# Optimization experiments

Measured on AMD Instinct MI355X. Metric: run time of the kernel, lower is better.

Reference implementation:

```python
import jax, jax.numpy as jnp
import numpy as np

B, L, C, D, K = 32, 36864, 16, 512, 24


def setup_inputs() -> dict:
    key = jax.random.key(0)
    ks = jax.random.split(key, 5)
    x = jax.random.normal(ks[0], (B, L, C), jnp.float32)
    # offset-conv weights scaled small so predicted offsets are O(0.2) (kaiming-ish but tame)
    w_off = jax.random.normal(ks[1], (2 * K, C, K), jnp.float32) * 0.01
    b_off = jax.random.normal(ks[2], (2 * K,), jnp.float32) * 0.05
    w_def = jax.random.normal(ks[3], (D, C, K), jnp.float32) * (2.0 / (C * K)) ** 0.5
    b_def = jax.random.normal(ks[4], (D,), jnp.float32) * 0.05
    return {"x": x, "w_off": w_off, "b_off": b_off, "w_def": w_def, "b_def": b_def}


def reference(x, w_off, b_off, w_def, b_def):
    # x: [B, L, C] -> torch view [B, C, 1, L]; H == 1 throughout.
    Bn, Ln, Cn = x.shape
    twoK, _, Kn = w_off.shape
    Lout = Ln // Kn
    xc = jnp.transpose(x, (0, 2, 1))                 # [B, C, L]
    xk = xc.reshape(Bn, Cn, Lout, Kn)                # stride == kernel -> non-overlapping windows
    # offset conv: [B, 2K, Lout]
    off = jnp.einsum('bclk,ock->bol', xk, w_off) + b_off[None, :, None]
    off = off.reshape(Bn, Kn, 2, Lout)               # channel 2k -> dy, 2k+1 -> dx (torchvision layout)
    dy = jnp.transpose(off[:, :, 0, :], (0, 2, 1))   # [B, Lout, K]
    dx = jnp.transpose(off[:, :, 1, :], (0, 2, 1))   # [B, Lout, K]
    # sampling positions along width; base = w_out*K + k
    base = jnp.arange(Lout * Kn, dtype=x.dtype).reshape(Lout, Kn)
    px = base[None] + dx                             # [B, Lout, K]
    # height bilinear weight: with H=1, contribution at h=0 is max(0, 1-|dy|)
    wy = jnp.maximum(jnp.array(0, x.dtype), 1.0 - jnp.abs(dy))
    # width bilinear with zero padding (torchvision bilinear_interpolate semantics)
    valid = (px > -1.0) & (px < Ln)
    x0 = jnp.floor(px)
    lw = px - x0                                     # weight for right neighbor
    i0 = x0.astype(jnp.int32)
    i1 = i0 + 1
    m0 = (valid & (i0 >= 0) & (i0 < Ln)).astype(x.dtype)
    m1 = (valid & (i1 >= 0) & (i1 < Ln)).astype(x.dtype)
    i0c = jnp.broadcast_to(jnp.clip(i0, 0, Ln - 1).reshape(Bn, 1, Lout * Kn), (Bn, Cn, Lout * Kn))
    i1c = jnp.broadcast_to(jnp.clip(i1, 0, Ln - 1).reshape(Bn, 1, Lout * Kn), (Bn, Cn, Lout * Kn))
    v0 = jnp.take_along_axis(xc, i0c, axis=2).reshape(Bn, Cn, Lout, Kn)
    v1 = jnp.take_along_axis(xc, i1c, axis=2).reshape(Bn, Cn, Lout, Kn)
    val = (v0 * ((1.0 - lw) * m0)[:, None] + v1 * (lw * m1)[:, None]) * wy[:, None]  # [B,C,Lout,K]
    out = jnp.einsum('bclk,dck->bld', val, w_def) + b_def  # [B, Lout, D]
    return out
```

## Files before the change

kernel.cpp:

```cpp
#include <hip/hip_runtime.h>
#include <stdint.h>

#define BATCH 32
#define LLEN  36864
#define CCH   16
#define DOUT  512
#define KW    24
#define LOUT  1536
#define MROWS (BATCH * LOUT)
#define CK    384
#define TWOK  48

typedef float fx4 __attribute__((ext_vector_type(4)));
typedef float f32x4 __attribute__((ext_vector_type(4)));
typedef __bf16 bf16x8 __attribute__((ext_vector_type(8)));
typedef uint32_t u32x4 __attribute__((ext_vector_type(4)));

#define VMCNT(n)  asm volatile("s_waitcnt vmcnt(" #n ")" ::: "memory")
#define LGKMCNT0  asm volatile("s_waitcnt lgkmcnt(0)" ::: "memory")
#define SCHEDB    __builtin_amdgcn_sched_barrier(0)
#define SBAR      __builtin_amdgcn_s_barrier()

__device__ __forceinline__ void gload16(void* lds, const void* g)
{
    __builtin_amdgcn_global_load_lds(
        (const __attribute__((address_space(1))) uint32_t*)g,
        (__attribute__((address_space(3))) uint32_t*)lds, 16, 0, 0);
}

__global__ __launch_bounds__(256) void prep_kernel(
    const float* __restrict__ w_off, const float* __restrict__ w_def,
    __bf16* __restrict__ woff_b, __bf16* __restrict__ wdef_b)
{
    int idx = blockIdx.x * 256 + threadIdx.x;
    if (idx < TWOK * CK) {
        int o = idx / CK, rem = idx % CK;
        int k = rem >> 4, c = rem & 15;
        woff_b[idx] = (__bf16)w_off[o * CK + c * KW + k];
    }
    if (idx < DOUT * CK) {
        int d = idx / CK, rem = idx % CK;
        int k = rem >> 4, c = rem & 15;
        wdef_b[idx] = (__bf16)w_def[d * CK + c * KW + k];
    }
}

#define BM 96
#define BN 512
#define BK 64

__global__ __launch_bounds__(512) void gemm_fused(
    const float* __restrict__ x, const __bf16* __restrict__ woff_b,
    const float* __restrict__ b_off, const __bf16* __restrict__ Bw,
    const float* __restrict__ bias, float* __restrict__ out)
{
    __shared__ char smem[77824];
    __bf16* As  = (__bf16*)smem;
    __bf16* Bs0 = (__bf16*)(smem + 12288);
    __bf16* Bs1 = (__bf16*)(smem + 45056);
    __bf16* WoffS = (__bf16*)smem;
    float*  offS  = (float*)(smem + 45056);

    const int t = threadIdx.x;
    const int m0 = blockIdx.x * BM;
    const int wave = t >> 6, lane = t & 63;
    const int quad = lane >> 4, l16 = lane & 15;
    const int wr = wave >> 2, wc = wave & 3;

    const int mloc = t >> 2, k4 = t & 3;
    const int Mrow = m0 + mloc;
    const int b    = m0 / LOUT;
    const int lb   = Mrow - b * LOUT;
    const float* xb = x + (size_t)b * LLEN * CCH;

#pragma unroll
    for (int i = 0; i < 5; ++i) {
        int q = t + 512 * i;
        if (q < 2304) {
            int row = q / 48, cc = q - row * 48;
            *(u32x4*)&WoffS[row * 392 + cc * 8] =
                *(const u32x4*)&woff_b[row * CK + cc * 8];
        }
    }
    __syncthreads();

    if (wave < 6) {
        const float* xr = x + (size_t)(m0 + wave * 16 + l16) * CK;
        f32x4 oacc[3] = {};
#pragma unroll
        for (int ks = 0; ks < 12; ++ks) {
            int k0 = ks * 32 + quad * 8;
            fx4 a0 = *(const fx4*)&xr[k0];
            fx4 a1 = *(const fx4*)&xr[k0 + 4];
            bf16x8 af;
            af[0] = (__bf16)a0.x; af[1] = (__bf16)a0.y;
            af[2] = (__bf16)a0.z; af[3] = (__bf16)a0.w;
            af[4] = (__bf16)a1.x; af[5] = (__bf16)a1.y;
            af[6] = (__bf16)a1.z; af[7] = (__bf16)a1.w;
#pragma unroll
            for (int j = 0; j < 3; ++j) {
                bf16x8 bf = *(const bf16x8*)&WoffS[(j * 16 + l16) * 392 + k0];
                oacc[j] = __builtin_amdgcn_mfma_f32_16x16x32_bf16(af, bf, oacc[j], 0, 0, 0);
            }
        }
        float bo[3];
#pragma unroll
        for (int j = 0; j < 3; ++j) bo[j] = b_off[j * 16 + l16];
#pragma unroll
        for (int j = 0; j < 3; ++j)
#pragma unroll
            for (int r = 0; r < 4; ++r)
                offS[(wave * 16 + quad * 4 + r) * 49 + j * 16 + l16] = oacc[j][r] + bo[j];
    }
    __syncthreads();

    uint32_t dxyr[6];
    if (t < 4 * BM) {
#pragma unroll
        for (int cc = 0; cc < 6; ++cc) {
            int kk = 4 * cc + k4;
            float dy = offS[mloc * 49 + 2 * kk];
            float dx = offS[mloc * 49 + 2 * kk + 1];
            union { __bf16 h[2]; uint32_t u; } p;
            p.h[0] = (__bf16)dy; p.h[1] = (__bf16)dx;
            dxyr[cc] = p.u;
        }
    }

    f32x4 acc[3][8] = {};
    fx4 g0[4], g1[4];
    float w0, w1;

    auto load_pair = [&](uint32_t pk, int kk) {
        union { uint32_t u; __bf16 h[2]; } p; p.u = pk;
        float dy = (float)p.h[0], dx = (float)p.h[1];
        float wy  = fmaxf(0.f, 1.f - fabsf(dy));
        float px  = (float)(lb * KW + kk) + dx;
        float x0f = floorf(px);
        float lw  = px - x0f;
        int   i0  = (int)x0f;
        bool valid = (px > -1.0f) && (px < (float)LLEN);
        w0 = (valid && i0 >= 0)         ? (1.f - lw) * wy : 0.f;
        w1 = (valid && (i0 + 1) < LLEN) ? lw * wy         : 0.f;
        int i0c = min(max(i0, 0), LLEN - 1);
        int i1c = min(max(i0 + 1, 0), LLEN - 1);
        const fx4* p0 = (const fx4*)&xb[(size_t)i0c * CCH];
        const fx4* p1 = (const fx4*)&xb[(size_t)i1c * CCH];
#pragma unroll
        for (int q = 0; q < 4; ++q) { g0[q] = p0[q]; g1[q] = p1[q]; }
    };

    auto dma_phase = [&](int ph, __bf16* buf) {
#pragma unroll
        for (int it = 0; it < 4; ++it) {
            int q = it * 512 + t;
            int c = q >> 2, s = q & 3;
            int ss = s ^ ((c >> 1) & 3);
            gload16(&buf[q * 8], Bw + (size_t)c * CK + ph * 32 + ss * 8);
        }
    };

    auto mfma_phase = [&](int ks, const __bf16* Bsb) {
        bf16x8 af[3], bfr[8];
#pragma unroll
        for (int i = 0; i < 3; ++i) {
            int row = wr * 48 + i * 16 + l16;
            af[i] = *(const bf16x8*)&As[row * BK + (((ks * 4 + quad) ^ (row & 7)) * 8)];
        }
#pragma unroll
        for (int j = 0; j < 8; ++j) {
            int col = wc * 128 + j * 16 + l16;
            bfr[j] = *(const bf16x8*)&Bsb[col * 32 + ((quad ^ ((col >> 1) & 3)) * 8)];
        }
#pragma unroll
        for (int i = 0; i < 3; ++i)
#pragma unroll
            for (int j = 0; j < 8; ++j)
                acc[i][j] = __builtin_amdgcn_mfma_f32_16x16x32_bf16(
                    af[i], bfr[j], acc[i][j], 0, 0, 0);
    };

    if (t < 4 * BM) load_pair(dxyr[0], k4);
    SCHEDB;
    dma_phase(0, Bs0);
    SCHEDB;

#pragma unroll
    for (int cc = 0; cc < 6; ++cc) {
        SBAR;
        SCHEDB;
        VMCNT(4);
        SCHEDB;
        if (t < 4 * BM) {
            bf16x8 oa, ob;
#pragma unroll
            for (int q = 0; q < 2; ++q) {
                fx4 v0 = g0[q], v1 = g1[q];
                oa[q * 4 + 0] = (__bf16)(w0 * v0.x + w1 * v1.x);
                oa[q * 4 + 1] = (__bf16)(w0 * v0.y + w1 * v1.y);
                oa[q * 4 + 2] = (__bf16)(w0 * v0.z + w1 * v1.z);
                oa[q * 4 + 3] = (__bf16)(w0 * v0.w + w1 * v1.w);
            }
#pragma unroll
            for (int q = 0; q < 2; ++q) {
                fx4 v0 = g0[q + 2], v1 = g1[q + 2];
                ob[q * 4 + 0] = (__bf16)(w0 * v0.x + w1 * v1.x);
                ob[q * 4 + 1] = (__bf16)(w0 * v0.y + w1 * v1.y);
                ob[q * 4 + 2] = (__bf16)(w0 * v0.z + w1 * v1.z);
                ob[q * 4 + 3] = (__bf16)(w0 * v0.w + w1 * v1.w);
            }
            int g = 2 * k4;
            *(bf16x8*)&As[mloc * BK + ((g ^ (mloc & 7)) * 8)]       = oa;
            *(bf16x8*)&As[mloc * BK + (((g + 1) ^ (mloc & 7)) * 8)] = ob;
        }
        SCHEDB;
        dma_phase(2 * cc + 1, Bs1);
        SCHEDB;
        if (cc + 1 < 6 && t < 4 * BM)
            load_pair(dxyr[cc + 1], 4 * (cc + 1) + k4);
        SCHEDB;
        LGKMCNT0;
        SCHEDB;
        SBAR;
        SCHEDB;
        if (cc < 5) { if (wave < 6) { VMCNT(12); } else { VMCNT(4); } }
        else        { VMCNT(4); }
        SCHEDB;
        SBAR;
        SCHEDB;
        __builtin_amdgcn_s_setprio(1);
        mfma_phase(0, Bs0);
        __builtin_amdgcn_s_setprio(0);
        SCHEDB;
        if (cc < 5) { if (wave < 6) { VMCNT(8); } else { VMCNT(0); } }
        else        { VMCNT(0); }
        SCHEDB;
        SBAR;
        SCHEDB;
        if (cc < 5) dma_phase(2 * cc + 2, Bs0);
        SCHEDB;
        __builtin_amdgcn_s_setprio(1);
        mfma_phase(1, Bs1);
        __builtin_amdgcn_s_setprio(0);
        SCHEDB;
    }

#pragma unroll
    for (int j = 0; j < 8; ++j) {
        int col = wc * 128 + j * 16 + l16;
        float bj = bias[col];
#pragma unroll
        for (int i = 0; i < 3; ++i) {
            int rowb = m0 + wr * 48 + i * 16 + quad * 4;
#pragma unroll
            for (int r = 0; r < 4; ++r)
                out[(size_t)(rowb + r) * DOUT + col] = acc[i][j][r] + bj;
        }
    }
}

extern "C" void kernel_launch(void* const* d_in, const int* in_sizes, int n_in,
                              void* d_out, int out_size, void* d_ws, size_t ws_size,
                              hipStream_t stream)
{
    const float* x     = (const float*)d_in[0];
    const float* w_off = (const float*)d_in[1];
    const float* b_off = (const float*)d_in[2];
    const float* w_def = (const float*)d_in[3];
    const float* b_def = (const float*)d_in[4];
    float* out = (float*)d_out;

    char* ws = (char*)d_ws;
    __bf16* wdef_b = (__bf16*)ws;
    __bf16* woff_b = (__bf16*)(ws + 393216);

    prep_kernel<<<768, 256, 0, stream>>>(w_off, w_def, woff_b, wdef_b);
    gemm_fused<<<MROWS / BM, 512, 0, stream>>>(x, woff_b, b_off, wdef_b, b_def, out);
}
```

Measured before the change: 194.4 us.

## Split fused deformable conv into gather kernel plus pipelined GEMM kernel

Replaces the single fused kernel with two kernels. The first computes the offsets with MFMA and writes the bilinearly gathered bf16 A matrix to workspace; the second is a double-buffered GEMM streaming A and the weights through LDS via global_load_lds. If the workspace is too small, the rows are processed in chunks. This separates the irregular gather from the GEMM main loop so each kernel can be scheduled for its own work, at the cost of an extra write and read of the A matrix through global memory and more kernel launches.

New measurement: 216.3 us. +11.3%, slower.

```diff
diff --git a/kernel.cpp b/kernel.cpp
--- a/kernel.cpp
+++ b/kernel.cpp
@@ -14,6 +14,7 @@
 typedef float fx4 __attribute__((ext_vector_type(4)));
 typedef float f32x4 __attribute__((ext_vector_type(4)));
 typedef __bf16 bf16x8 __attribute__((ext_vector_type(8)));
+typedef __bf16 bf16x4 __attribute__((ext_vector_type(4)));
 typedef uint32_t u32x4 __attribute__((ext_vector_type(4)));
 
 #define VMCNT(n)  asm volatile("s_waitcnt vmcnt(" #n ")" ::: "memory")
@@ -48,6 +49,205 @@
 #define BM 96
 #define BN 512
 #define BK 64
+
+
+__global__ __launch_bounds__(384) void k1_gather(
+    const float* __restrict__ x, const __bf16* __restrict__ woff_b,
+    const float* __restrict__ b_off, __bf16* __restrict__ A_ws, int mbase)
+{
+    __shared__ char smem[37632];
+    __bf16* WoffS = (__bf16*)smem;
+    float*  offS  = (float*)smem;
+
+    const int t = threadIdx.x;
+    const int mrel0 = blockIdx.x * BM;
+    const int m0 = mbase + mrel0;
+    const int wave = t >> 6, lane = t & 63;
+    const int quad = lane >> 4, l16 = lane & 15;
+
+    const int mloc = t >> 2, k4 = t & 3;
+    const int Mrow = m0 + mloc;
+    const int mrel = mrel0 + mloc;
+    const int b    = m0 / LOUT;
+    const int lb   = Mrow - b * LOUT;
+    const float* xb = x + (size_t)b * LLEN * CCH;
+
+#pragma unroll
+    for (int i = 0; i < 6; ++i) {
+        int q = t + 384 * i;
+        int row = q / 48, cc = q - row * 48;
+        *(u32x4*)&WoffS[row * 392 + cc * 8] =
+            *(const u32x4*)&woff_b[row * CK + cc * 8];
+    }
+    __syncthreads();
+
+    const float* xr = x + (size_t)(m0 + wave * 16 + l16) * CK;
+    f32x4 oacc[3] = {};
+#pragma unroll
+    for (int ks = 0; ks < 12; ++ks) {
+        int k0 = ks * 32 + quad * 8;
+        fx4 a0 = *(const fx4*)&xr[k0];
+        fx4 a1 = *(const fx4*)&xr[k0 + 4];
+        bf16x8 af;
+        af[0] = (__bf16)a0.x; af[1] = (__bf16)a0.y;
+        af[2] = (__bf16)a0.z; af[3] = (__bf16)a0.w;
+        af[4] = (__bf16)a1.x; af[5] = (__bf16)a1.y;
+        af[6] = (__bf16)a1.z; af[7] = (__bf16)a1.w;
+#pragma unroll
+        for (int j = 0; j < 3; ++j) {
+            bf16x8 bf = *(const bf16x8*)&WoffS[(j * 16 + l16) * 392 + k0];
+            oacc[j] = __builtin_amdgcn_mfma_f32_16x16x32_bf16(af, bf, oacc[j], 0, 0, 0);
+        }
+    }
+    float bo[3];
+#pragma unroll
+    for (int j = 0; j < 3; ++j) bo[j] = b_off[j * 16 + l16];
+    __syncthreads();
+#pragma unroll
+    for (int j = 0; j < 3; ++j)
+#pragma unroll
+        for (int r = 0; r < 4; ++r)
+            offS[(wave * 16 + quad * 4 + r) * 49 + j * 16 + l16] = oacc[j][r] + bo[j];
+    __syncthreads();
+
+    float dyv[6], dxv[6];
+#pragma unroll
+    for (int cc = 0; cc < 6; ++cc) {
+        int kk = 4 * cc + k4;
+        dyv[cc] = offS[mloc * 49 + 2 * kk];
+        dxv[cc] = offS[mloc * 49 + 2 * kk + 1];
+    }
+
+    for (int cc = 0; cc < 6; ++cc) {
+        int kk = 4 * cc + k4;
+        float dy = dyv[cc], dx = dxv[cc];
+        float wy  = fmaxf(0.f, 1.f - fabsf(dy));
+        float px  = (float)(lb * KW + kk) + dx;
+        float x0f = floorf(px);
+        float lw  = px - x0f;
+        int   i0  = (int)x0f;
+        bool valid = (px > -1.0f) && (px < (float)LLEN);
+        float w0 = (valid && i0 >= 0)         ? (1.f - lw) * wy : 0.f;
+        float w1 = (valid && (i0 + 1) < LLEN) ? lw * wy         : 0.f;
+        int i0c = min(max(i0, 0), LLEN - 1);
+        int i1c = min(max(i0 + 1, 0), LLEN - 1);
+        const fx4* p0 = (const fx4*)&xb[(size_t)i0c * CCH];
+        const fx4* p1 = (const fx4*)&xb[(size_t)i1c * CCH];
+        fx4 g0[4], g1[4];
+#pragma unroll
+        for (int q = 0; q < 4; ++q) { g0[q] = p0[q]; g1[q] = p1[q]; }
+        bf16x8 oa, ob;
+#pragma unroll
+        for (int q = 0; q < 2; ++q) {
+            fx4 v0 = g0[q], v1 = g1[q];
+            oa[q * 4 + 0] = (__bf16)(w0 * v0.x + w1 * v1.x);
+            oa[q * 4 + 1] = (__bf16)(w0 * v0.y + w1 * v1.y);
+            oa[q * 4 + 2] = (__bf16)(w0 * v0.z + w1 * v1.z);
+            oa[q * 4 + 3] = (__bf16)(w0 * v0.w + w1 * v1.w);
+        }
+#pragma unroll
+        for (int q = 0; q < 2; ++q) {
+            fx4 v0 = g0[q + 2], v1 = g1[q + 2];
+            ob[q * 4 + 0] = (__bf16)(w0 * v0.x + w1 * v1.x);
+            ob[q * 4 + 1] = (__bf16)(w0 * v0.y + w1 * v1.y);
+            ob[q * 4 + 2] = (__bf16)(w0 * v0.z + w1 * v1.z);
+            ob[q * 4 + 3] = (__bf16)(w0 * v0.w + w1 * v1.w);
+        }
+        __bf16* dst = A_ws + (size_t)mrel * CK + kk * 16;
+        *(bf16x8*)dst       = oa;
+        *(bf16x8*)(dst + 8) = ob;
+    }
+}
+
+__global__ __launch_bounds__(512) void k2_gemm(
+    const __bf16* __restrict__ A_ws, const __bf16* __restrict__ Bw,
+    const float* __restrict__ bias, float* __restrict__ out, int mbase)
+{
+    __shared__ char smem[77824];
+    __bf16* As0 = (__bf16*)smem;
+    __bf16* As1 = (__bf16*)(smem + 6144);
+    __bf16* Bs0 = (__bf16*)(smem + 12288);
+    __bf16* Bs1 = (__bf16*)(smem + 45056);
+
+    const int t = threadIdx.x;
+    const int mrel0 = blockIdx.x * BM;
+    const int wave = t >> 6, lane = t & 63;
+    const int quad = lane >> 4, l16 = lane & 15;
+    const int wr = wave >> 2, wc = wave & 3;
+
+    auto dma = [&](int p, __bf16* AsB, __bf16* BsB) {
+#pragma unroll
+        for (int it = 0; it < 4; ++it) {
+            int q = it * 512 + t;
+            int c = q >> 2, s = q & 3;
+            int ss = s ^ ((c >> 1) & 3);
+            gload16(&BsB[q * 8], Bw + (size_t)c * CK + p * 32 + ss * 8);
+        }
+        if (t < 384) {
+            int row = t >> 2, g = t & 3;
+            int gg = g ^ ((row >> 1) & 3);
+            gload16(&AsB[t * 8],
+                    A_ws + (size_t)(mrel0 + row) * CK + p * 32 + gg * 8);
+        }
+    };
+
+    f32x4 acc[3][8] = {};
+
+    auto mfma_phase = [&](const __bf16* AsB, const __bf16* BsB) {
+        bf16x8 af[3], bfr[8];
+#pragma unroll
+        for (int i = 0; i < 3; ++i) {
+            int row = wr * 48 + i * 16 + l16;
+            af[i] = *(const bf16x8*)&AsB[row * 32 + ((quad ^ ((row >> 1) & 3)) * 8)];
+        }
+#pragma unroll
+        for (int j = 0; j < 8; ++j) {
+            int col = wc * 128 + j * 16 + l16;
+            bfr[j] = *(const bf16x8*)&BsB[col * 32 + ((quad ^ ((col >> 1) & 3)) * 8)];
+        }
+#pragma unroll
+        for (int i = 0; i < 3; ++i)
+#pragma unroll
+            for (int j = 0; j < 8; ++j)
+                acc[i][j] = __builtin_amdgcn_mfma_f32_16x16x32_bf16(
+                    af[i], bfr[j], acc[i][j], 0, 0, 0);
+    };
+
+    dma(0, As0, Bs0);
+#pragma unroll
+    for (int p = 0; p < 12; ++p) {
+        __bf16* Ac = (p & 1) ? As1 : As0;
+        __bf16* Bc = (p & 1) ? Bs1 : Bs0;
+        __bf16* An = (p & 1) ? As0 : As1;
+        __bf16* Bn = (p & 1) ? Bs0 : Bs1;
+        if (p < 11) dma(p + 1, An, Bn);
+        SCHEDB;
+        if (p < 11) { if (wave < 6) { VMCNT(5); } else { VMCNT(4); } }
+        else        { VMCNT(0); }
+        SCHEDB;
+        SBAR;
+        SCHEDB;
+        __builtin_amdgcn_s_setprio(1);
+        mfma_phase(Ac, Bc);
+        __builtin_amdgcn_s_setprio(0);
+        SCHEDB;
+        SBAR;
+        SCHEDB;
+    }
+
+#pragma unroll
+    for (int j = 0; j < 8; ++j) {
+        int col = wc * 128 + j * 16 + l16;
+        float bj = bias[col];
+#pragma unroll
+        for (int i = 0; i < 3; ++i) {
+            int rowb = mbase + mrel0 + wr * 48 + i * 16 + quad * 4;
+#pragma unroll
+            for (int r = 0; r < 4; ++r)
+                out[(size_t)(rowb + r) * DOUT + col] = acc[i][j][r] + bj;
+        }
+    }
+}
 
 __global__ __launch_bounds__(512) void gemm_fused(
     const float* __restrict__ x, const __bf16* __restrict__ woff_b,
@@ -273,7 +473,24 @@
     char* ws = (char*)d_ws;
     __bf16* wdef_b = (__bf16*)ws;
     __bf16* woff_b = (__bf16*)(ws + 393216);
+    __bf16* A_ws   = (__bf16*)(ws + 430080);
 
     prep_kernel<<<768, 256, 0, stream>>>(w_off, w_def, woff_b, wdef_b);
-    gemm_fused<<<MROWS / BM, 512, 0, stream>>>(x, woff_b, b_off, wdef_b, b_def, out);
-}
+
+    const size_t afull = (size_t)MROWS * CK * 2;
+    int S = -1;
+    for (int s = 1; s <= 32; s <<= 1) {
+        if (430080 + afull / s <= ws_size) { S = s; break; }
+    }
+    if (S > 0) {
+        int rows = MROWS / S;
+        int nb   = rows / BM;
+        for (int c = 0; c < S; ++c) {
+            int mb = c * rows;
+            k1_gather<<<nb, 384, 0, stream>>>(x, woff_b, b_off, A_ws, mb);
+            k2_gemm<<<nb, 512, 0, stream>>>(A_ws, wdef_b, b_def, out, mb);
+        }
+    } else {
+        gemm_fused<<<MROWS / BM, 512, 0, stream>>>(x, woff_b, b_off, wdef_b, b_def, out);
+    }
+}
```
